# Kernel tuning notes

Hardware: AMD Instinct MI355X
Metric: run time of the kernel (lower is better)

The kernel has to match this reference:

```python
import jax, jax.numpy as jnp
import numpy as np

R = 32  # reduced channel dim = outplane // reduction
TRI_I, TRI_J = np.triu_indices(R)  # static upper-triangle indices (528 pairs)


def setup_inputs() -> dict:
    key = jax.random.key(0)
    k1, k2, k3 = jax.random.split(key, 3)
    B, Cin, H, W = 8, 256, 96, 96
    Cout = 256
    tri = R * (R + 1) // 2  # 528
    x = jax.random.normal(k1, (B, Cin, H, W), dtype=jnp.float32)
    # 1x1 conv weights stored as [out, in] matrices
    w_reduce = jax.random.normal(k2, (R, Cin), dtype=jnp.float32) * (1.0 / np.sqrt(Cin))
    w_recover = jax.random.normal(k3, (Cout, tri), dtype=jnp.float32) * (1.0 / np.sqrt(tri))
    return {"x": x, "w_reduce": w_reduce, "w_recover": w_recover}


def reference(x, w_reduce, w_recover):
    # reduce: 1x1 conv (no bias): [B,Cin,H,W] -> [B,R,H,W]
    out = jnp.einsum('bchw,rc->brhw', x, w_reduce)
    # per-pixel outer product, but only the upper-triangle entries:
    # bilinear[b,i,j,h,w] = out[b,i,h,w] * out[b,j,h,w]; gather (i,j) in triu
    i = jnp.asarray(TRI_I)
    j = jnp.asarray(TRI_J)
    up = out[:, i, :, :] * out[:, j, :, :]  # [B, 528, H, W]
    # channelRecover: 1x1 conv 528 -> Cout
    y = jnp.einsum('bthw,ot->bohw', up, w_recover)
    # signed sqrt
    return jnp.sign(y) * jnp.sqrt(jnp.abs(y) + 1e-6)
```

## Files before the change

kernel.cpp:

```cpp
#include <hip/hip_runtime.h>
#include <hip/hip_bf16.h>
#include <math.h>

#define HW     9216
#define CIN    256
#define RCH    32
#define NTRI   528
#define COUT   256
#define NB     8
#define W16ROW 544
#define UROW   40
#define XROW2  40

typedef _Float16 f16x8 __attribute__((ext_vector_type(8)));
typedef _Float16 f16x4 __attribute__((ext_vector_type(4)));
typedef float    f32x4 __attribute__((ext_vector_type(4)));

__global__ __launch_bounds__(256) void convert_kernel(
    const float* __restrict__ w_reduce, const float* __restrict__ w_recover,
    _Float16* __restrict__ w16, _Float16* __restrict__ wr16h,
    _Float16* __restrict__ wr16l) {
  const int bx = blockIdx.x;
  const int tid = threadIdx.x;
  if (bx < COUT) {
    for (int t = tid; t < W16ROW; t += 256) {
      float f = (t < NTRI) ? w_recover[(size_t)bx * NTRI + t] : 0.0f;
      w16[(size_t)bx * W16ROW + t] = (_Float16)f;
    }
  } else {
    int e = (bx - COUT) * 512 + tid;
#pragma unroll
    for (int k = 0; k < 2; ++k, e += 256) {
      float f = w_reduce[e];
      _Float16 h = (_Float16)f;
      wr16h[e] = h;
      wr16l[e] = (_Float16)(f - (float)h);
    }
  }
}

__global__ __launch_bounds__(256, 4) void fused_kernel(
    const float* __restrict__ x, const _Float16* __restrict__ w16,
    const _Float16* __restrict__ wr16h, const _Float16* __restrict__ wr16l,
    float* __restrict__ y) {
  __shared__ float outS[RCH * 68];
  __shared__ short triI[NTRI];
  __shared__ short triJ[NTRI];
  __shared__ __align__(16) union {
    struct { _Float16 xh[2][64 * XROW2]; _Float16 xl[2][64 * XROW2]; } g1;
    struct { _Float16 up[2][64 * UROW]; } g2;
  } su;

  const int tid = threadIdx.x;
  const int bx = blockIdx.x;
  const int b  = bx / 144;
  const int p0 = (bx - b * 144) * 64;

  const int wv   = tid >> 6;
  const int lane = tid & 63;
  const int ml   = lane & 15;
  const int q    = lane >> 4;

  for (int t = tid; t < NTRI; t += 256) {
    float disc = 4225.0f - 8.0f * (float)t;
    int i = (int)floorf((65.0f - sqrtf(disc)) * 0.5f);
    while ((i + 1) * (65 - (i + 1)) / 2 <= t) ++i;
    while (i * (65 - i) / 2 > t) --i;
    triI[t] = (short)i;
    triJ[t] = (short)(i + t - i * (65 - i) / 2);
  }

  {
    f32x4 g1acc[2];
#pragma unroll
    for (int mt = 0; mt < 2; ++mt)
#pragma unroll
      for (int r2 = 0; r2 < 4; ++r2) g1acc[mt][r2] = 0.0f;

    const int c4 = (tid & 7) * 4;
    const int p2 = (tid >> 3) * 2;
    for (int ch = 0; ch < 8; ++ch) {
      const int cur = ch & 1;
      const int c0 = ch * 32;
      f16x8 ah[2], al[2];
#pragma unroll
      for (int mt = 0; mt < 2; ++mt) {
        const int off = (mt * 16 + ml) * CIN + c0 + q * 8;
        ah[mt] = *(const f16x8*)&wr16h[off];
        al[mt] = *(const f16x8*)&wr16l[off];
      }
      float v[4][2];
#pragma unroll
      for (int i2 = 0; i2 < 4; ++i2) {
        float2 xv = *(const float2*)&x[((size_t)(b * CIN + c0 + c4 + i2)) * HW + p0 + p2];
        v[i2][0] = xv.x; v[i2][1] = xv.y;
      }
#pragma unroll
      for (int jp = 0; jp < 2; ++jp) {
        f16x4 hi, lo;
#pragma unroll
        for (int i2 = 0; i2 < 4; ++i2) {
          float f = v[i2][jp];
          _Float16 h = (_Float16)f;
          hi[i2] = h;
          lo[i2] = (_Float16)(f - (float)h);
        }
        *(f16x4*)&su.g1.xh[cur][(p2 + jp) * XROW2 + c4] = hi;
        *(f16x4*)&su.g1.xl[cur][(p2 + jp) * XROW2 + c4] = lo;
      }
      __syncthreads();
      f16x8 bh = *(const f16x8*)&su.g1.xh[cur][(wv * 16 + ml) * XROW2 + q * 8];
      f16x8 bl = *(const f16x8*)&su.g1.xl[cur][(wv * 16 + ml) * XROW2 + q * 8];
#pragma unroll
      for (int mt = 0; mt < 2; ++mt) {
        g1acc[mt] = __builtin_amdgcn_mfma_f32_16x16x32_f16(ah[mt], bh, g1acc[mt], 0, 0, 0);
        g1acc[mt] = __builtin_amdgcn_mfma_f32_16x16x32_f16(al[mt], bh, g1acc[mt], 0, 0, 0);
        g1acc[mt] = __builtin_amdgcn_mfma_f32_16x16x32_f16(ah[mt], bl, g1acc[mt], 0, 0, 0);
      }
    }
#pragma unroll
    for (int mt = 0; mt < 2; ++mt)
#pragma unroll
      for (int reg = 0; reg < 4; ++reg)
        outS[(mt * 16 + q * 4 + reg) * 68 + wv * 16 + ml] = g1acc[mt][reg];
  }
  __syncthreads();

  f32x4 acc[4][4];
#pragma unroll
  for (int mi = 0; mi < 4; ++mi)
#pragma unroll
    for (int ni = 0; ni < 4; ++ni)
#pragma unroll
      for (int r2 = 0; r2 < 4; ++r2) acc[mi][ni][r2] = 0.0f;

  const int u_p = lane;
  const int u_g = wv;

  for (int chunk = 0; chunk < 17; ++chunk) {
    const int cur = chunk & 1;
    const int t0 = chunk * 32;
    f16x8 afr[4];
#pragma unroll
    for (int mi = 0; mi < 4; ++mi)
      afr[mi] = *(const f16x8*)&w16[(size_t)(wv * 64 + mi * 16 + ml) * W16ROW + t0 + q * 8];
    {
      f16x8 uv8;
#pragma unroll
      for (int s = 0; s < 8; ++s) {
        int t = t0 + u_g * 8 + s;
        float v = 0.0f;
        if (t < NTRI) {
          int i = triI[t];
          int j = triJ[t];
          v = outS[i * 68 + u_p] * outS[j * 68 + u_p];
        }
        uv8[s] = (_Float16)v;
      }
      *(f16x8*)&su.g2.up[cur][u_p * UROW + u_g * 8] = uv8;
    }
    __syncthreads();
    f16x8 bfr[4];
#pragma unroll
    for (int ni = 0; ni < 4; ++ni)
      bfr[ni] = *(const f16x8*)&su.g2.up[cur][(ni * 16 + ml) * UROW + q * 8];
#pragma unroll
    for (int mi = 0; mi < 4; ++mi)
#pragma unroll
      for (int ni = 0; ni < 4; ++ni)
        acc[mi][ni] = __builtin_amdgcn_mfma_f32_16x16x32_f16(afr[mi], bfr[ni], acc[mi][ni], 0, 0, 0);
  }

#pragma unroll
  for (int mi = 0; mi < 4; ++mi) {
#pragma unroll
    for (int reg = 0; reg < 4; ++reg) {
      const int o = wv * 64 + mi * 16 + q * 4 + reg;
      float* yrow = y + ((size_t)(b * COUT + o)) * HW + p0 + ml;
#pragma unroll
      for (int ni = 0; ni < 4; ++ni) {
        float v = acc[mi][ni][reg];
        float s = sqrtf(fabsf(v) + 1e-6f);
        yrow[ni * 16] = v > 0.0f ? s : (v < 0.0f ? -s : 0.0f);
      }
    }
  }
}

extern "C" void kernel_launch(void* const* d_in, const int* in_sizes, int n_in,
                              void* d_out, int out_size, void* d_ws, size_t ws_size,
                              hipStream_t stream) {
  const float* x         = (const float*)d_in[0];
  const float* w_reduce  = (const float*)d_in[1];
  const float* w_recover = (const float*)d_in[2];
  float* y = (float*)d_out;

  _Float16* w16   = (_Float16*)d_ws;
  _Float16* wr16h = (_Float16*)((char*)d_ws + 278528);
  _Float16* wr16l = (_Float16*)((char*)d_ws + 278528 + 16384);

  convert_kernel<<<COUT + 16, 256, 0, stream>>>(w_reduce, w_recover, w16, wr16h, wr16l);
  fused_kernel<<<NB * (HW / 64), 256, 0, stream>>>(x, w16, wr16h, wr16l, y);
}
```

Baseline: 192.6 us.

## Build bilinear tile in two halves with compile-time triangle indices

```diff
diff --git a/kernel.cpp b/kernel.cpp
--- a/kernel.cpp
+++ b/kernel.cpp
@@ -9,12 +9,52 @@
 #define COUT   256
 #define NB     8
 #define W16ROW 544
-#define UROW   40
-#define XROW2  40
+#define UPROW  296
 
 typedef _Float16 f16x8 __attribute__((ext_vector_type(8)));
-typedef _Float16 f16x4 __attribute__((ext_vector_type(4)));
 typedef float    f32x4 __attribute__((ext_vector_type(4)));
+
+struct TriTab { unsigned char i[544]; unsigned char j[544]; };
+constexpr TriTab make_tri() {
+  TriTab t{};
+  int ii = 0, jj = 0;
+  for (int k = 0; k < 544; ++k) {
+    if (k < NTRI) {
+      t.i[k] = (unsigned char)ii; t.j[k] = (unsigned char)jj;
+      if (++jj == 32) { ++ii; jj = ii; }
+    } else { t.i[k] = 0; t.j[k] = 0; }
+  }
+  return t;
+}
+constexpr TriTab TRI = make_tri();
+
+template<int TQ, int HALF>
+__device__ __forceinline__ void build_up(const float (&o)[RCH], _Float16* rowp) {
+  constexpr int NG  = HALF ? 8 : 9;
+  constexpr int TLB = TQ * (HALF ? 64 : 72);
+  constexpr int TB  = HALF ? 288 : 0;
+#pragma unroll
+  for (int g = 0; g < NG; ++g) {
+    f16x8 v;
+#pragma unroll
+    for (int s = 0; s < 8; ++s) {
+      const int tl = TLB + g * 8 + s;
+      const int t  = TB + tl;
+      float f = (t < NTRI) ? o[TRI.i[t]] * o[TRI.j[t]] : 0.0f;
+      v[s] = (_Float16)f;
+    }
+    *(f16x8*)&rowp[TLB + g * 8] = v;
+  }
+}
+
+template<int HALF>
+__device__ __forceinline__ void build_dispatch(int wv, const float (&o)[RCH],
+                                               _Float16* rowp) {
+  if (wv == 0)      build_up<0, HALF>(o, rowp);
+  else if (wv == 1) build_up<1, HALF>(o, rowp);
+  else if (wv == 2) build_up<2, HALF>(o, rowp);
+  else              build_up<3, HALF>(o, rowp);
+}
 
 __global__ __launch_bounds__(256) void convert_kernel(
     const float* __restrict__ w_reduce, const float* __restrict__ w_recover,
@@ -39,37 +79,22 @@
   }
 }
 
-__global__ __launch_bounds__(256, 4) void fused_kernel(
+__global__ __launch_bounds__(256, 3) void fused_kernel(
     const float* __restrict__ x, const _Float16* __restrict__ w16,
     const _Float16* __restrict__ wr16h, const _Float16* __restrict__ wr16l,
     float* __restrict__ y) {
   __shared__ float outS[RCH * 68];
-  __shared__ short triI[NTRI];
-  __shared__ short triJ[NTRI];
-  __shared__ __align__(16) union {
-    struct { _Float16 xh[2][64 * XROW2]; _Float16 xl[2][64 * XROW2]; } g1;
-    struct { _Float16 up[2][64 * UROW]; } g2;
-  } su;
-
-  const int tid = threadIdx.x;
-  const int bx = blockIdx.x;
-  const int b  = bx / 144;
-  const int p0 = (bx - b * 144) * 64;
-
+  __shared__ __align__(16) _Float16 upS[64 * UPROW];
+
+  const int tid  = threadIdx.x;
+  const int bx   = blockIdx.x;
+  const int b    = bx / 144;
+  const int p0   = (bx - b * 144) * 64;
   const int wv   = tid >> 6;
   const int lane = tid & 63;
   const int ml   = lane & 15;
   const int q    = lane >> 4;
 
-  for (int t = tid; t < NTRI; t += 256) {
-    float disc = 4225.0f - 8.0f * (float)t;
-    int i = (int)floorf((65.0f - sqrtf(disc)) * 0.5f);
-    while ((i + 1) * (65 - (i + 1)) / 2 <= t) ++i;
-    while (i * (65 - i) / 2 > t) --i;
-    triI[t] = (short)i;
-    triJ[t] = (short)(i + t - i * (65 - i) / 2);
-  }
-
   {
     f32x4 g1acc[2];
 #pragma unroll
@@ -77,45 +102,29 @@
 #pragma unroll
       for (int r2 = 0; r2 < 4; ++r2) g1acc[mt][r2] = 0.0f;
 
-    const int c4 = (tid & 7) * 4;
-    const int p2 = (tid >> 3) * 2;
+    const float* xb = x + (size_t)b * CIN * HW + p0 + wv * 16 + ml;
+#pragma unroll
     for (int ch = 0; ch < 8; ++ch) {
-      const int cur = ch & 1;
       const int c0 = ch * 32;
-      f16x8 ah[2], al[2];
+      float xv[8];
+#pragma unroll
+      for (int s = 0; s < 8; ++s)
+        xv[s] = xb[(size_t)(c0 + q * 8 + s) * HW];
+      f16x8 bh, bl;
+#pragma unroll
+      for (int s = 0; s < 8; ++s) {
+        _Float16 h = (_Float16)xv[s];
+        bh[s] = h;
+        bl[s] = (_Float16)(xv[s] - (float)h);
+      }
 #pragma unroll
       for (int mt = 0; mt < 2; ++mt) {
         const int off = (mt * 16 + ml) * CIN + c0 + q * 8;
-        ah[mt] = *(const f16x8*)&wr16h[off];
-        al[mt] = *(const f16x8*)&wr16l[off];
-      }
-      float v[4][2];
-#pragma unroll
-      for (int i2 = 0; i2 < 4; ++i2) {
-        float2 xv = *(const float2*)&x[((size_t)(b * CIN + c0 + c4 + i2)) * HW + p0 + p2];
-        v[i2][0] = xv.x; v[i2][1] = xv.y;
-      }
-#pragma unroll
-      for (int jp = 0; jp < 2; ++jp) {
-        f16x4 hi, lo;
-#pragma unroll
-        for (int i2 = 0; i2 < 4; ++i2) {
-          float f = v[i2][jp];
-          _Float16 h = (_Float16)f;
-          hi[i2] = h;
-          lo[i2] = (_Float16)(f - (float)h);
-        }
-        *(f16x4*)&su.g1.xh[cur][(p2 + jp) * XROW2 + c4] = hi;
-        *(f16x4*)&su.g1.xl[cur][(p2 + jp) * XROW2 + c4] = lo;
-      }
-      __syncthreads();
-      f16x8 bh = *(const f16x8*)&su.g1.xh[cur][(wv * 16 + ml) * XROW2 + q * 8];
-      f16x8 bl = *(const f16x8*)&su.g1.xl[cur][(wv * 16 + ml) * XROW2 + q * 8];
-#pragma unroll
-      for (int mt = 0; mt < 2; ++mt) {
-        g1acc[mt] = __builtin_amdgcn_mfma_f32_16x16x32_f16(ah[mt], bh, g1acc[mt], 0, 0, 0);
-        g1acc[mt] = __builtin_amdgcn_mfma_f32_16x16x32_f16(al[mt], bh, g1acc[mt], 0, 0, 0);
-        g1acc[mt] = __builtin_amdgcn_mfma_f32_16x16x32_f16(ah[mt], bl, g1acc[mt], 0, 0, 0);
+        f16x8 ah = *(const f16x8*)&wr16h[off];
+        f16x8 al = *(const f16x8*)&wr16l[off];
+        g1acc[mt] = __builtin_amdgcn_mfma_f32_16x16x32_f16(ah, bh, g1acc[mt], 0, 0, 0);
+        g1acc[mt] = __builtin_amdgcn_mfma_f32_16x16x32_f16(al, bh, g1acc[mt], 0, 0, 0);
+        g1acc[mt] = __builtin_amdgcn_mfma_f32_16x16x32_f16(ah, bl, g1acc[mt], 0, 0, 0);
       }
     }
 #pragma unroll
@@ -134,36 +143,53 @@
 #pragma unroll
       for (int r2 = 0; r2 < 4; ++r2) acc[mi][ni][r2] = 0.0f;
 
-  const int u_p = lane;
-  const int u_g = wv;
-
-  for (int chunk = 0; chunk < 17; ++chunk) {
-    const int cur = chunk & 1;
-    const int t0 = chunk * 32;
+  _Float16* rowp = &upS[lane * UPROW];
+
+  {
+    float o[RCH];
+#pragma unroll
+    for (int r = 0; r < RCH; ++r) o[r] = outS[r * 68 + lane];
+    build_dispatch<0>(wv, o, rowp);
+  }
+  __syncthreads();
+#pragma unroll
+  for (int c = 0; c < 9; ++c) {
+    const int t0 = c * 32;
     f16x8 afr[4];
 #pragma unroll
     for (int mi = 0; mi < 4; ++mi)
       afr[mi] = *(const f16x8*)&w16[(size_t)(wv * 64 + mi * 16 + ml) * W16ROW + t0 + q * 8];
-    {
-      f16x8 uv8;
-#pragma unroll
-      for (int s = 0; s < 8; ++s) {
-        int t = t0 + u_g * 8 + s;
-        float v = 0.0f;
-        if (t < NTRI) {
-          int i = triI[t];
-          int j = triJ[t];
-          v = outS[i * 68 + u_p] * outS[j * 68 + u_p];
-        }
-        uv8[s] = (_Float16)v;
-      }
-      *(f16x8*)&su.g2.up[cur][u_p * UROW + u_g * 8] = uv8;
-    }
-    __syncthreads();
     f16x8 bfr[4];
 #pragma unroll
     for (int ni = 0; ni < 4; ++ni)
-      bfr[ni] = *(const f16x8*)&su.g2.up[cur][(ni * 16 + ml) * UROW + q * 8];
+      bfr[ni] = *(const f16x8*)&upS[(ni * 16 + ml) * UPROW + t0 + q * 8];
+#pragma unroll
+    for (int mi = 0; mi < 4; ++mi)
+#pragma unroll
+      for (int ni = 0; ni < 4; ++ni)
+        acc[mi][ni] = __builtin_amdgcn_mfma_f32_16x16x32_f16(afr[mi], bfr[ni], acc[mi][ni], 0, 0, 0);
+  }
+  __syncthreads();
+
+  {
+    float o[RCH];
+#pragma unroll
+    for (int r = 0; r < RCH; ++r) o[r] = outS[r * 68 + lane];
+    build_dispatch<1>(wv, o, rowp);
+  }
+  __syncthreads();
+#pragma unroll
+  for (int c = 0; c < 8; ++c) {
+    const int t0l = c * 32;
+    const int t0g = 288 + c * 32;
+    f16x8 afr[4];
+#pragma unroll
+    for (int mi = 0; mi < 4; ++mi)
+      afr[mi] = *(const f16x8*)&w16[(size_t)(wv * 64 + mi * 16 + ml) * W16ROW + t0g + q * 8];
+    f16x8 bfr[4];
+#pragma unroll
+    for (int ni = 0; ni < 4; ++ni)
+      bfr[ni] = *(const f16x8*)&upS[(ni * 16 + ml) * UPROW + t0l + q * 8];
 #pragma unroll
     for (int mi = 0; mi < 4; ++mi)
 #pragma unroll
```

Result: faster. 179.4 us (-6.9%).
